# Kernel tuning notes

Hardware: AMD Instinct MI355X
Metric: run time of the kernel (lower is better)

Reference implementation:

```python
import jax, jax.numpy as jnp
import numpy as np

H = 256      # hidden_dim
ID = 512     # image_dim
TD = 512     # text_dim
NC = 80      # num_classes
NH = 4       # attention heads
HD = H // NH # head dim
B = 131072


def setup_inputs() -> dict:
    key = jax.random.key(0)
    ks = jax.random.split(key, 30)
    def rn(k, shape, scale=0.02):
        return jax.random.normal(k, shape, jnp.float32) * scale
    img = jax.random.normal(ks[0], (B, ID), jnp.float32)
    txt = jax.random.normal(ks[1], (B, TD), jnp.float32)
    r = jax.random.uniform(ks[2], (B,))
    img = img * (r >= 0.15).astype(jnp.float32)[:, None]
    txt = txt * (~((r >= 0.15) & (r < 0.30))).astype(jnp.float32)[:, None]
    return {
        'image_features': img,
        'text_features': txt,
        'W_ie': rn(ks[3], (ID, H)), 'b_ie': jnp.zeros((H,), jnp.float32),
        'W_te': rn(ks[4], (TD, H)), 'b_te': jnp.zeros((H,), jnp.float32),
        'fusion_query': rn(ks[5], (1, 1, H)),
        'Wq': rn(ks[6], (H, H)), 'bq': jnp.zeros((H,), jnp.float32),
        'Wk': rn(ks[7], (H, H)), 'bk': jnp.zeros((H,), jnp.float32),
        'Wv': rn(ks[8], (H, H)), 'bv': jnp.zeros((H,), jnp.float32),
        'Wo': rn(ks[9], (H, H)), 'bo': jnp.zeros((H,), jnp.float32),
        'W_ip': rn(ks[10], (H, 2 * H)), 'b_ip': jnp.zeros((2 * H,), jnp.float32),
        'W_tp': rn(ks[11], (H, 2 * H)), 'b_tp': jnp.zeros((2 * H,), jnp.float32),
        'W_fp': rn(ks[12], (H, 2 * H)), 'b_fp': jnp.zeros((2 * H,), jnp.float32),
        'Wc1': rn(ks[13], (2 * H, H)), 'bc1': jnp.zeros((H,), jnp.float32),
        'Wc2': rn(ks[14], (H, NC)), 'bc2': jnp.zeros((NC,), jnp.float32),
    }


def reference(image_features, text_features, W_ie, b_ie, W_te, b_te,
              fusion_query, Wq, bq, Wk, bk, Wv, bv, Wo, bo,
              W_ip, b_ip, W_tp, b_tp, W_fp, b_fp, Wc1, bc1, Wc2, bc2):
    # encoders (dropout inactive in eval)
    img_enc = jax.nn.relu(image_features @ W_ie + b_ie)   # [B,H]
    txt_enc = jax.nn.relu(text_features @ W_te + b_te)    # [B,H]

    img_present = jnp.linalg.norm(image_features, axis=1) > 1e-6
    txt_present = jnp.linalg.norm(text_features, axis=1) > 1e-6
    both = img_present & txt_present
    only_img = img_present & ~txt_present
    only_txt = ~img_present & txt_present

    # fusion branch: MHA pooling, query len 1, kv = two stacked modalities
    kv = jnp.stack([img_enc, txt_enc], axis=1)             # [B,2,H]
    q = (fusion_query.reshape(1, H) @ Wq + bq).reshape(NH, HD)      # [h,d]
    k = (kv @ Wk + bk).reshape(-1, 2, NH, HD)              # [B,2,h,d]
    v = (kv @ Wv + bv).reshape(-1, 2, NH, HD)
    scores = jnp.einsum('hd,bshd->bhs', q, k) / np.sqrt(HD)
    attn = jax.nn.softmax(scores, axis=-1)                 # [B,h,2]
    pooled = jnp.einsum('bhs,bshd->bhd', attn, v).reshape(-1, H)
    pooled = pooled @ Wo + bo                              # [B,H]
    fusion_out = pooled @ W_fp + b_fp                      # [B,2H]

    img_out = img_enc @ W_ip + b_ip                        # [B,2H]
    txt_out = txt_enc @ W_tp + b_tp                        # [B,2H]

    zero = jnp.zeros_like(fusion_out)
    fused = jnp.where(both[:, None], fusion_out,
            jnp.where(only_img[:, None], img_out,
            jnp.where(only_txt[:, None], txt_out, zero)))

    logits = jax.nn.relu(fused @ Wc1 + bc1) @ Wc2 + bc2    # [B,NC]
    return logits
```

## Files before the change

### kernel.cpp

```cpp
#include <hip/hip_runtime.h>
#include <hip/hip_fp16.h>
#include <math.h>

constexpr int H   = 256;
constexpr int ID  = 512;
constexpr int NC  = 80;
constexpr int BT  = 131072;

constexpr int MROWS = 32;
constexpr int NBLK  = BT / MROWS;

typedef _Float16 half8  __attribute__((ext_vector_type(8)));
typedef float    floatx4 __attribute__((ext_vector_type(4)));

#define MFMA16(a,b,c) __builtin_amdgcn_mfma_f32_16x16x32_f16((a),(b),(c),0,0,0)

__device__ inline half8 splat8(_Float16 v){ half8 r = {v,v,v,v,v,v,v,v}; return r; }

__device__ __align__(16) _Float16 g_WieT[H*ID];
__device__ __align__(16) _Float16 g_WteT[H*ID];
__device__ __align__(16) _Float16 g_WvT [H*H];
__device__ __align__(16) _Float16 g_WipT[2*H*H];
__device__ __align__(16) _Float16 g_WtpT[2*H*H];
__device__ __align__(16) _Float16 g_WofT[2*H*H];
__device__ __align__(16) _Float16 g_Wc1T[H*2*H];
__device__ __align__(16) _Float16 g_Wc2T[NC*H];
__device__ __align__(16) float g_wkeff[4*H];
__device__ float g_sbias[4];
__device__ float g_biasof[2*H];

constexpr int OFF_EI = 0;
constexpr int OFF_ET = 8448;
constexpr int OFF_PL = 16896;
constexpr int OFF_SUMI = 50688;
constexpr int OFF_SUMT = 51200;
constexpr int OFF_ATT  = 51712;
constexpr int OFF_SELB = 52736;
constexpr int OFF_SELI = 52864;
constexpr int OFF_SELT = 52992;
constexpr int SMEM_BYTES = 53120;

__global__ void aecf_setup(const float* __restrict__ W_ie, const float* __restrict__ W_te,
                           const float* __restrict__ fq,   const float* __restrict__ Wq,
                           const float* __restrict__ bq,   const float* __restrict__ Wk,
                           const float* __restrict__ bk,   const float* __restrict__ Wv,
                           const float* __restrict__ Wo,   const float* __restrict__ bo,
                           const float* __restrict__ W_ip, const float* __restrict__ W_tp,
                           const float* __restrict__ W_fp, const float* __restrict__ b_fp,
                           const float* __restrict__ Wc1,  const float* __restrict__ Wc2)
{
    __shared__ float qv[256];
    int b = blockIdx.x, t = threadIdx.x;

    if (b < 512) { int e = b*256+t; int k=e>>8, n=e&255; g_WieT[n*512+k] = (_Float16)W_ie[e]; return; }
    b -= 512;
    if (b < 512) { int e = b*256+t; int k=e>>8, n=e&255; g_WteT[n*512+k] = (_Float16)W_te[e]; return; }
    b -= 512;
    if (b < 256) { int e = b*256+t; int k=e>>8, n=e&255; g_WvT[n*256+k] = (_Float16)Wv[e]; return; }
    b -= 256;
    if (b < 512) { int e = b*256+t; int k=e>>9, n=e&511; g_WipT[n*256+k] = (_Float16)W_ip[e]; return; }
    b -= 512;
    if (b < 512) { int e = b*256+t; int k=e>>9, n=e&511; g_WtpT[n*256+k] = (_Float16)W_tp[e]; return; }
    b -= 512;
    if (b < 512) { int e = b*256+t; int k=e>>8, n=e&255; g_Wc1T[n*512+k] = (_Float16)Wc1[e]; return; }
    b -= 512;
    if (b < 80)  { int e = b*256+t; int k=e/80, n=e%80;  g_Wc2T[n*256+k] = (_Float16)Wc2[e]; return; }
    b -= 80;
    if (b < 512) {
        int n = b, c = t;
        float s = 0.f;
        for (int m = 0; m < 256; m++) s += Wo[c*256+m] * W_fp[m*512+n];
        g_WofT[n*256+c] = (_Float16)s;
        return;
    }
    b -= 512;
    if (b == 0) {
        float a = bq[t];
        for (int i = 0; i < 256; i++) a += fq[i] * Wq[i*256+t];
        qv[t] = a;
        __syncthreads();
        for (int h = 0; h < 4; h++) {
            float s = 0.f;
            for (int d = 0; d < 64; d++) s += Wk[t*256 + h*64+d] * qv[h*64+d];
            g_wkeff[h*256 + t] = s * 0.125f;
        }
        if (t < 4) {
            float s = 0.f;
            for (int d = 0; d < 64; d++) s += bk[t*64+d] * qv[t*64+d];
            g_sbias[t] = s * 0.125f;
        }
        return;
    }
    b -= 1;
    {
        int n = b*256 + t;
        float s = b_fp[n];
        for (int m = 0; m < 256; m++) s += bo[m] * W_fp[m*512+n];
        g_biasof[n] = s;
    }
}

__global__ __launch_bounds__(256, 3)
void aecf_main(const float* __restrict__ img, const float* __restrict__ txt,
               const float* __restrict__ b_ie, const float* __restrict__ b_te,
               const float* __restrict__ bv,   const float* __restrict__ b_ip,
               const float* __restrict__ b_tp, const float* __restrict__ bc1,
               const float* __restrict__ bc2,  float* __restrict__ out)
{
    extern __shared__ char smem[];
    _Float16* encI  = (_Float16*)smem + OFF_EI;
    _Float16* encT  = (_Float16*)smem + OFF_ET;
    _Float16* pool  = (_Float16*)smem + OFF_PL;
    _Float16* fused = (_Float16*)smem;
    _Float16* h1    = pool;
    float* sumI = (float*)(smem + OFF_SUMI);
    float* sumT = (float*)(smem + OFF_SUMT);
    float* attn = (float*)(smem + OFF_ATT);
    float* selb = (float*)(smem + OFF_SELB);
    float* seli = (float*)(smem + OFF_SELI);
    float* selt = (float*)(smem + OFF_SELT);

    const int tid  = threadIdx.x;
    const int w    = tid >> 6;
    const int lane = tid & 63;
    const int l16  = lane & 15;
    const int q4   = lane >> 4;
    const int base = blockIdx.x * MROWS;

    auto encode = [&](const float* __restrict__ src, const _Float16* __restrict__ WT,
                      const float* __restrict__ bias, _Float16* dstE, float* sumLds) {
        floatx4 acc[2][4];
        #pragma unroll
        for (int rt = 0; rt < 2; rt++)
            #pragma unroll
            for (int ct = 0; ct < 4; ct++) acc[rt][ct] = (floatx4){0.f,0.f,0.f,0.f};
        float sab[2] = {0.f, 0.f};

        for (int ks = 0; ks < 16; ks++) {
            const int k0 = ks*32 + q4*8;
            half8 afr[2];
            #pragma unroll
            for (int rt = 0; rt < 2; rt++) {
                const float* p = src + (size_t)(base + rt*16 + l16)*ID + k0;
                floatx4 x0 = *(const floatx4*)p;
                floatx4 x1 = *(const floatx4*)(p+4);
                half8 a;
                a[0]=(_Float16)x0[0]; a[1]=(_Float16)x0[1]; a[2]=(_Float16)x0[2]; a[3]=(_Float16)x0[3];
                a[4]=(_Float16)x1[0]; a[5]=(_Float16)x1[1]; a[6]=(_Float16)x1[2]; a[7]=(_Float16)x1[3];
                afr[rt] = a;
                if (w == 0)
                    sab[rt] += fabsf(x0[0])+fabsf(x0[1])+fabsf(x0[2])+fabsf(x0[3])
                             + fabsf(x1[0])+fabsf(x1[1])+fabsf(x1[2])+fabsf(x1[3]);
            }
            #pragma unroll
            for (int ct = 0; ct < 4; ct++) {
                const int ng = w*64 + ct*16 + l16;
                half8 bfr = *(const half8*)(WT + (size_t)ng*512 + k0);
                #pragma unroll
                for (int rt = 0; rt < 2; rt++) acc[rt][ct] = MFMA16(afr[rt], bfr, acc[rt][ct]);
            }
        }
        #pragma unroll
        for (int ct = 0; ct < 4; ct++) {
            const int colg = w*64 + ct*16 + l16;
            const float bb = bias[colg];
            #pragma unroll
            for (int rt = 0; rt < 2; rt++)
                #pragma unroll
                for (int r = 0; r < 4; r++) {
                    float v = acc[rt][ct][r] + bb;
                    v = v > 0.f ? v : 0.f;
                    dstE[(rt*16 + q4*4 + r)*264 + colg] = (_Float16)v;
                }
        }
        if (w == 0) {
            #pragma unroll
            for (int rt = 0; rt < 2; rt++) sumLds[(rt*16 + l16)*4 + q4] = sab[rt];
        }
    };
    encode(img, g_WieT, b_ie, encI, sumI);
    encode(txt, g_WteT, b_te, encT, sumT);
    __syncthreads();

    if (tid < 128) {
        const int row = tid >> 2, h = tid & 3;
        float sI = sumI[row*4]+sumI[row*4+1]+sumI[row*4+2]+sumI[row*4+3];
        float sT = sumT[row*4]+sumT[row*4+1]+sumT[row*4+2]+sumT[row*4+3];
        bool pi = sI > 0.f, pt = sT > 0.f;
        if (h == 0) {
            selb[row] = (pi && pt)  ? 1.f : 0.f;
            seli[row] = (pi && !pt) ? 1.f : 0.f;
            selt[row] = (!pi && pt) ? 1.f : 0.f;
        }
        float s0 = g_sbias[h], s1 = s0;
        const _Float16* rI = encI + row*264;
        const _Float16* rT = encT + row*264;
        const float* wkh = g_wkeff + h*256;
        for (int c8 = 0; c8 < 256; c8 += 8) {
            half8 eI = *(const half8*)(rI + c8);
            half8 eT = *(const half8*)(rT + c8);
            floatx4 wa = *(const floatx4*)(wkh + c8);
            floatx4 wb = *(const floatx4*)(wkh + c8 + 4);
            s0 += wa[0]*(float)eI[0] + wa[1]*(float)eI[1] + wa[2]*(float)eI[2] + wa[3]*(float)eI[3]
                + wb[0]*(float)eI[4] + wb[1]*(float)eI[5] + wb[2]*(float)eI[6] + wb[3]*(float)eI[7];
            s1 += wa[0]*(float)eT[0] + wa[1]*(float)eT[1] + wa[2]*(float)eT[2] + wa[3]*(float)eT[3]
                + wb[0]*(float)eT[4] + wb[1]*(float)eT[5] + wb[2]*(float)eT[6] + wb[3]*(float)eT[7];
        }
        const float a0 = 1.f / (1.f + __expf(s1 - s0));
        attn[(row*4+h)*2]   = a0;
        attn[(row*4+h)*2+1] = 1.f - a0;
    }
    __syncthreads();

    {
        floatx4 poolacc[4][2];
        #pragma unroll
        for (int h = 0; h < 4; h++)
            #pragma unroll
            for (int rt = 0; rt < 2; rt++) poolacc[h][rt] = (floatx4){0.f,0.f,0.f,0.f};

        #pragma unroll
        for (int h = 0; h < 4; h++) {
            _Float16 a0l[2], a1l[2];
            #pragma unroll
            for (int rt = 0; rt < 2; rt++) {
                const int rr = rt*16 + l16;
                a0l[rt] = (_Float16)attn[(rr*4+h)*2];
                a1l[rt] = (_Float16)attn[(rr*4+h)*2+1];
            }
            const int ng = h*64 + w*16 + l16;
            for (int ks = 0; ks < 8; ks++) {
                const int k0 = ks*32 + q4*8;
                half8 bfr = *(const half8*)(g_WvT + (size_t)ng*256 + k0);
                #pragma unroll
                for (int rt = 0; rt < 2; rt++) {
                    half8 eI = *(const half8*)(encI + (rt*16+l16)*264 + k0);
                    half8 eT = *(const half8*)(encT + (rt*16+l16)*264 + k0);
                    half8 m  = eI * splat8(a0l[rt]) + eT * splat8(a1l[rt]);
                    poolacc[h][rt] = MFMA16(m, bfr, poolacc[h][rt]);
                }
            }
        }
        #pragma unroll
        for (int h = 0; h < 4; h++) {
            const int colg = h*64 + w*16 + l16;
            const float bvv = bv[colg];
            #pragma unroll
            for (int rt = 0; rt < 2; rt++)
                #pragma unroll
                for (int r = 0; r < 4; r++) {
                    const int row = rt*16 + q4*4 + r;
                    pool[row*264 + colg] = (_Float16)((poolacc[h][rt][r] + bvv) * selb[row]);
                }
        }
    }
    __syncthreads();

    floatx4 pacc[2][8];
    #pragma unroll
    for (int rt = 0; rt < 2; rt++)
        #pragma unroll
        for (int ct = 0; ct < 8; ct++) pacc[rt][ct] = (floatx4){0.f,0.f,0.f,0.f};

    {
        _Float16 s[2];
        #pragma unroll
        for (int rt = 0; rt < 2; rt++) s[rt] = (_Float16)seli[rt*16 + l16];
        for (int ks = 0; ks < 8; ks++) {
            const int k0 = ks*32 + q4*8;
            half8 afr[2];
            #pragma unroll
            for (int rt = 0; rt < 2; rt++)
                afr[rt] = (*(const half8*)(encI + (rt*16+l16)*264 + k0)) * splat8(s[rt]);
            #pragma unroll
            for (int ct = 0; ct < 8; ct++) {
                const int ng = w*128 + ct*16 + l16;
                half8 bfr = *(const half8*)(g_WipT + (size_t)ng*256 + k0);
                #pragma unroll
                for (int rt = 0; rt < 2; rt++) pacc[rt][ct] = MFMA16(afr[rt], bfr, pacc[rt][ct]);
            }
        }
    }
    {
        _Float16 s[2];
        #pragma unroll
        for (int rt = 0; rt < 2; rt++) s[rt] = (_Float16)selt[rt*16 + l16];
        for (int ks = 0; ks < 8; ks++) {
            const int k0 = ks*32 + q4*8;
            half8 afr[2];
            #pragma unroll
            for (int rt = 0; rt < 2; rt++)
                afr[rt] = (*(const half8*)(encT + (rt*16+l16)*264 + k0)) * splat8(s[rt]);
            #pragma unroll
            for (int ct = 0; ct < 8; ct++) {
                const int ng = w*128 + ct*16 + l16;
                half8 bfr = *(const half8*)(g_WtpT + (size_t)ng*256 + k0);
                #pragma unroll
                for (int rt = 0; rt < 2; rt++) pacc[rt][ct] = MFMA16(afr[rt], bfr, pacc[rt][ct]);
            }
        }
    }
    {
        for (int ks = 0; ks < 8; ks++) {
            const int k0 = ks*32 + q4*8;
            half8 afr[2];
            #pragma unroll
            for (int rt = 0; rt < 2; rt++)
                afr[rt] = *(const half8*)(pool + (rt*16+l16)*264 + k0);
            #pragma unroll
            for (int ct = 0; ct < 8; ct++) {
                const int ng = w*128 + ct*16 + l16;
                half8 bfr = *(const half8*)(g_WofT + (size_t)ng*256 + k0);
                #pragma unroll
                for (int rt = 0; rt < 2; rt++) pacc[rt][ct] = MFMA16(afr[rt], bfr, pacc[rt][ct]);
            }
        }
    }
    __syncthreads();

    {
        float sB[8], sI2[8], sT2[8];
        #pragma unroll
        for (int rt = 0; rt < 2; rt++)
            #pragma unroll
            for (int r = 0; r < 4; r++) {
                const int row = rt*16 + q4*4 + r;
                sB[rt*4+r] = selb[row]; sI2[rt*4+r] = seli[row]; sT2[rt*4+r] = selt[row];
            }
        #pragma unroll
        for (int ct = 0; ct < 8; ct++) {
            const int colg = w*128 + ct*16 + l16;
            const float bof = g_biasof[colg], bip = b_ip[colg], btp = b_tp[colg];
            #pragma unroll
            for (int rt = 0; rt < 2; rt++)
                #pragma unroll
                for (int r = 0; r < 4; r++) {
                    const int row = rt*16 + q4*4 + r;
                    const float f = pacc[rt][ct][r] + sB[rt*4+r]*bof + sI2[rt*4+r]*bip + sT2[rt*4+r]*btp;
                    fused[row*520 + colg] = (_Float16)f;
                }
        }
    }
    __syncthreads();

    {
        floatx4 cacc[2][4];
        #pragma unroll
        for (int rt = 0; rt < 2; rt++)
            #pragma unroll
            for (int ct = 0; ct < 4; ct++) cacc[rt][ct] = (floatx4){0.f,0.f,0.f,0.f};
        for (int ks = 0; ks < 16; ks++) {
            const int k0 = ks*32 + q4*8;
            half8 afr[2];
            #pragma unroll
            for (int rt = 0; rt < 2; rt++)
                afr[rt] = *(const half8*)(fused + (rt*16+l16)*520 + k0);
            #pragma unroll
            for (int ct = 0; ct < 4; ct++) {
                const int ng = w*64 + ct*16 + l16;
                half8 bfr = *(const half8*)(g_Wc1T + (size_t)ng*512 + k0);
                #pragma unroll
                for (int rt = 0; rt < 2; rt++) cacc[rt][ct] = MFMA16(afr[rt], bfr, cacc[rt][ct]);
            }
        }
        __syncthreads();
        #pragma unroll
        for (int ct = 0; ct < 4; ct++) {
            const int colg = w*64 + ct*16 + l16;
            const float b1 = bc1[colg];
            #pragma unroll
            for (int rt = 0; rt < 2; rt++)
                #pragma unroll
                for (int r = 0; r < 4; r++) {
                    float v = cacc[rt][ct][r] + b1;
                    v = v > 0.f ? v : 0.f;
                    h1[(rt*16 + q4*4 + r)*264 + colg] = (_Float16)v;
                }
        }
    }
    __syncthreads();

    for (int p = w; p < 10; p += 4) {
        const int rt = p / 5, ct = p % 5;
        const int ng = ct*16 + l16;
        floatx4 a2 = (floatx4){0.f,0.f,0.f,0.f};
        for (int ks = 0; ks < 8; ks++) {
            const int k0 = ks*32 + q4*8;
            half8 afr = *(const half8*)(h1 + (rt*16+l16)*264 + k0);
            half8 bfr = *(const half8*)(g_Wc2T + (size_t)ng*256 + k0);
            a2 = MFMA16(afr, bfr, a2);
        }
        const float b2 = bc2[ng];
        #pragma unroll
        for (int r = 0; r < 4; r++) {
            const int rowg = base + rt*16 + q4*4 + r;
            out[(size_t)rowg*NC + ng] = a2[r] + b2;
        }
    }
}

extern "C" void kernel_launch(void* const* d_in, const int* in_sizes, int n_in,
                              void* d_out, int out_size, void* d_ws, size_t ws_size,
                              hipStream_t stream)
{
    const float* img  = (const float*)d_in[0];
    const float* txt  = (const float*)d_in[1];
    const float* W_ie = (const float*)d_in[2];
    const float* b_ie = (const float*)d_in[3];
    const float* W_te = (const float*)d_in[4];
    const float* b_te = (const float*)d_in[5];
    const float* fq   = (const float*)d_in[6];
    const float* Wq   = (const float*)d_in[7];
    const float* bq   = (const float*)d_in[8];
    const float* Wk   = (const float*)d_in[9];
    const float* bk   = (const float*)d_in[10];
    const float* Wv   = (const float*)d_in[11];
    const float* bv   = (const float*)d_in[12];
    const float* Wo   = (const float*)d_in[13];
    const float* bo   = (const float*)d_in[14];
    const float* W_ip = (const float*)d_in[15];
    const float* b_ip = (const float*)d_in[16];
    const float* W_tp = (const float*)d_in[17];
    const float* b_tp = (const float*)d_in[18];
    const float* W_fp = (const float*)d_in[19];
    const float* b_fp = (const float*)d_in[20];
    const float* Wc1  = (const float*)d_in[21];
    const float* bc1  = (const float*)d_in[22];
    const float* Wc2  = (const float*)d_in[23];
    const float* bc2  = (const float*)d_in[24];
    float* out = (float*)d_out;

    hipFuncSetAttribute((const void*)aecf_main,
                        hipFuncAttributeMaxDynamicSharedMemorySize, SMEM_BYTES);

    aecf_setup<<<3411, 256, 0, stream>>>(W_ie, W_te, fq, Wq, bq, Wk, bk, Wv,
                                         Wo, bo, W_ip, W_tp, W_fp, b_fp, Wc1, Wc2);
    aecf_main<<<NBLK, 256, SMEM_BYTES, stream>>>(img, txt, b_ie, b_te, bv,
                                                 b_ip, b_tp, bc1, bc2, out);
}
```

Baseline: 1.661 ms.

## Alias pool buffer onto text encodings, reorder pooling, prefetch encoder inputs

Result: slower. 2.000 ms (+20.4%).

```diff
diff --git a/kernel.cpp b/kernel.cpp
--- a/kernel.cpp
+++ b/kernel.cpp
@@ -31,14 +31,13 @@
 
 constexpr int OFF_EI = 0;
 constexpr int OFF_ET = 8448;
-constexpr int OFF_PL = 16896;
-constexpr int OFF_SUMI = 50688;
-constexpr int OFF_SUMT = 51200;
-constexpr int OFF_ATT  = 51712;
-constexpr int OFF_SELB = 52736;
-constexpr int OFF_SELI = 52864;
-constexpr int OFF_SELT = 52992;
-constexpr int SMEM_BYTES = 53120;
+constexpr int OFF_SUMI = 33792;
+constexpr int OFF_SUMT = 34304;
+constexpr int OFF_ATT  = 34816;
+constexpr int OFF_SELB = 35840;
+constexpr int OFF_SELI = 35968;
+constexpr int OFF_SELT = 36096;
+constexpr int SMEM_BYTES = 36224;
 
 __global__ void aecf_setup(const float* __restrict__ W_ie, const float* __restrict__ W_te,
                            const float* __restrict__ fq,   const float* __restrict__ Wq,
@@ -100,7 +99,7 @@
     }
 }
 
-__global__ __launch_bounds__(256, 3)
+__global__ __launch_bounds__(256, 4)
 void aecf_main(const float* __restrict__ img, const float* __restrict__ txt,
                const float* __restrict__ b_ie, const float* __restrict__ b_te,
                const float* __restrict__ bv,   const float* __restrict__ b_ip,
@@ -110,9 +109,9 @@
     extern __shared__ char smem[];
     _Float16* encI  = (_Float16*)smem + OFF_EI;
     _Float16* encT  = (_Float16*)smem + OFF_ET;
-    _Float16* pool  = (_Float16*)smem + OFF_PL;
+    _Float16* pool  = (_Float16*)smem + OFF_ET;
     _Float16* fused = (_Float16*)smem;
-    _Float16* h1    = pool;
+    _Float16* h1    = (_Float16*)smem;
     float* sumI = (float*)(smem + OFF_SUMI);
     float* sumT = (float*)(smem + OFF_SUMT);
     float* attn = (float*)(smem + OFF_ATT);
@@ -136,21 +135,34 @@
             for (int ct = 0; ct < 4; ct++) acc[rt][ct] = (floatx4){0.f,0.f,0.f,0.f};
         float sab[2] = {0.f, 0.f};
 
+        const float* p0 = src + (size_t)(base + l16)*ID + q4*8;
+        const float* p1 = src + (size_t)(base + 16 + l16)*ID + q4*8;
+        floatx4 n00 = *(const floatx4*)p0, n01 = *(const floatx4*)(p0+4);
+        floatx4 n10 = *(const floatx4*)p1, n11 = *(const floatx4*)(p1+4);
+
         for (int ks = 0; ks < 16; ks++) {
             const int k0 = ks*32 + q4*8;
             half8 afr[2];
-            #pragma unroll
-            for (int rt = 0; rt < 2; rt++) {
-                const float* p = src + (size_t)(base + rt*16 + l16)*ID + k0;
-                floatx4 x0 = *(const floatx4*)p;
-                floatx4 x1 = *(const floatx4*)(p+4);
+            {
                 half8 a;
-                a[0]=(_Float16)x0[0]; a[1]=(_Float16)x0[1]; a[2]=(_Float16)x0[2]; a[3]=(_Float16)x0[3];
-                a[4]=(_Float16)x1[0]; a[5]=(_Float16)x1[1]; a[6]=(_Float16)x1[2]; a[7]=(_Float16)x1[3];
-                afr[rt] = a;
-                if (w == 0)
-                    sab[rt] += fabsf(x0[0])+fabsf(x0[1])+fabsf(x0[2])+fabsf(x0[3])
-                             + fabsf(x1[0])+fabsf(x1[1])+fabsf(x1[2])+fabsf(x1[3]);
+                a[0]=(_Float16)n00[0]; a[1]=(_Float16)n00[1]; a[2]=(_Float16)n00[2]; a[3]=(_Float16)n00[3];
+                a[4]=(_Float16)n01[0]; a[5]=(_Float16)n01[1]; a[6]=(_Float16)n01[2]; a[7]=(_Float16)n01[3];
+                afr[0] = a;
+                half8 c;
+                c[0]=(_Float16)n10[0]; c[1]=(_Float16)n10[1]; c[2]=(_Float16)n10[2]; c[3]=(_Float16)n10[3];
+                c[4]=(_Float16)n11[0]; c[5]=(_Float16)n11[1]; c[6]=(_Float16)n11[2]; c[7]=(_Float16)n11[3];
+                afr[1] = c;
+            }
+            if (w == 0) {
+                sab[0] += fabsf(n00[0])+fabsf(n00[1])+fabsf(n00[2])+fabsf(n00[3])
+                        + fabsf(n01[0])+fabsf(n01[1])+fabsf(n01[2])+fabsf(n01[3]);
+                sab[1] += fabsf(n10[0])+fabsf(n10[1])+fabsf(n10[2])+fabsf(n10[3])
+                        + fabsf(n11[0])+fabsf(n11[1])+fabsf(n11[2])+fabsf(n11[3]);
+            }
+            if (ks < 15) {
+                const int kn = (ks+1)*32;
+                n00 = *(const floatx4*)(p0 + kn);  n01 = *(const floatx4*)(p0 + kn + 4);
+                n10 = *(const floatx4*)(p1 + kn);  n11 = *(const floatx4*)(p1 + kn + 4);
             }
             #pragma unroll
             for (int ct = 0; ct < 4; ct++) {
@@ -212,50 +224,6 @@
     }
     __syncthreads();
 
-    {
-        floatx4 poolacc[4][2];
-        #pragma unroll
-        for (int h = 0; h < 4; h++)
-            #pragma unroll
-            for (int rt = 0; rt < 2; rt++) poolacc[h][rt] = (floatx4){0.f,0.f,0.f,0.f};
-
-        #pragma unroll
-        for (int h = 0; h < 4; h++) {
-            _Float16 a0l[2], a1l[2];
-            #pragma unroll
-            for (int rt = 0; rt < 2; rt++) {
-                const int rr = rt*16 + l16;
-                a0l[rt] = (_Float16)attn[(rr*4+h)*2];
-                a1l[rt] = (_Float16)attn[(rr*4+h)*2+1];
-            }
-            const int ng = h*64 + w*16 + l16;
-            for (int ks = 0; ks < 8; ks++) {
-                const int k0 = ks*32 + q4*8;
-                half8 bfr = *(const half8*)(g_WvT + (size_t)ng*256 + k0);
-                #pragma unroll
-                for (int rt = 0; rt < 2; rt++) {
-                    half8 eI = *(const half8*)(encI + (rt*16+l16)*264 + k0);
-                    half8 eT = *(const half8*)(encT + (rt*16+l16)*264 + k0);
-                    half8 m  = eI * splat8(a0l[rt]) + eT * splat8(a1l[rt]);
-                    poolacc[h][rt] = MFMA16(m, bfr, poolacc[h][rt]);
-                }
-            }
-        }
-        #pragma unroll
-        for (int h = 0; h < 4; h++) {
-            const int colg = h*64 + w*16 + l16;
-            const float bvv = bv[colg];
-            #pragma unroll
-            for (int rt = 0; rt < 2; rt++)
-                #pragma unroll
-                for (int r = 0; r < 4; r++) {
-                    const int row = rt*16 + q4*4 + r;
-                    pool[row*264 + colg] = (_Float16)((poolacc[h][rt][r] + bvv) * selb[row]);
-                }
-        }
-    }
-    __syncthreads();
-
     floatx4 pacc[2][8];
     #pragma unroll
     for (int rt = 0; rt < 2; rt++)
@@ -300,6 +268,51 @@
             }
         }
     }
+
+    floatx4 poolacc[4][2];
+    #pragma unroll
+    for (int h = 0; h < 4; h++)
+        #pragma unroll
+        for (int rt = 0; rt < 2; rt++) poolacc[h][rt] = (floatx4){0.f,0.f,0.f,0.f};
+
+    #pragma unroll
+    for (int h = 0; h < 4; h++) {
+        _Float16 a0l[2], a1l[2];
+        #pragma unroll
+        for (int rt = 0; rt < 2; rt++) {
+            const int rr = rt*16 + l16;
+            a0l[rt] = (_Float16)attn[(rr*4+h)*2];
+            a1l[rt] = (_Float16)attn[(rr*4+h)*2+1];
+        }
+        const int ng = h*64 + w*16 + l16;
+        for (int ks = 0; ks < 8; ks++) {
+            const int k0 = ks*32 + q4*8;
+            half8 bfr = *(const half8*)(g_WvT + (size_t)ng*256 + k0);
+            #pragma unroll
+            for (int rt = 0; rt < 2; rt++) {
+                half8 eI = *(const half8*)(encI + (rt*16+l16)*264 + k0);
+                half8 eT = *(const half8*)(encT + (rt*16+l16)*264 + k0);
+                half8 m  = eI * splat8(a0l[rt]) + eT * splat8(a1l[rt]);
+                poolacc[h][rt] = MFMA16(m, bfr, poolacc[h][rt]);
+            }
+        }
+    }
+    __syncthreads();
+
+    #pragma unroll
+    for (int h = 0; h < 4; h++) {
+        const int colg = h*64 + w*16 + l16;
+        const float bvv = bv[colg];
+        #pragma unroll
+        for (int rt = 0; rt < 2; rt++)
+            #pragma unroll
+            for (int r = 0; r < 4; r++) {
+                const int row = rt*16 + q4*4 + r;
+                pool[row*264 + colg] = (_Float16)((poolacc[h][rt][r] + bvv) * selb[row]);
+            }
+    }
+    __syncthreads();
+
     {
         for (int ks = 0; ks < 8; ks++) {
             const int k0 = ks*32 + q4*8;
```
